# Optimization experiments

Measured on AMD Instinct MI355X. Metric: run time of the kernel, lower is better.

Reference implementation:

```python
import jax, jax.numpy as jnp
import numpy as np
from jax.scipy.special import logsumexp

B, T, V, E, F, H, L = 64, 512, 30000, 256, 256, 256, 9
DROPOUT_RATE, DROPOUT_ROUND = 0.1, 4


def setup_inputs() -> dict:
    key = jax.random.key(0)
    ks = jax.random.split(key, 20)
    lengths = jax.random.randint(ks[0], (B,), T // 2, T + 1)
    tok = jax.random.randint(ks[1], (B, T), 1, V)
    input_ids = jnp.where(jnp.arange(T)[None, :] < lengths[:, None], tok, 0).astype(jnp.int32)
    labels = jax.random.randint(ks[2], (B, T), 0, L).astype(jnp.int32)
    W_emb = (jax.random.normal(ks[3], (V, E)) * 0.1).at[0].set(0.0)  # padding_idx=0 row zeroed
    w0 = jax.random.normal(ks[4], (F, F, 3)) * 0.05
    w1 = jax.random.normal(ks[5], (F, F, 3)) * 0.05
    w2 = jax.random.normal(ks[6], (F, F, 3)) * 0.05
    Wl = jax.random.normal(ks[7], (E, F)) * 0.05
    Wh = jax.random.normal(ks[8], (F, H)) * 0.05
    Wfc = jax.random.normal(ks[9], (H, L)) * 0.05
    crf_start = jax.random.normal(ks[10], (L,)) * 0.1
    crf_end = jax.random.normal(ks[11], (L,)) * 0.1
    crf_trans = jax.random.normal(ks[12], (L, L)) * 0.1
    z = jnp.zeros
    return dict(input_ids=input_ids, labels=labels, W_emb=W_emb,
                w0=w0, b0=z((F,)), w1=w1, b1=z((F,)), w2=w2, b2=z((F,)),
                Wl=Wl, bl=z((F,)), Wh=Wh, bh=z((H,)), Wfc=Wfc, bfc=z((L,)),
                crf_start=crf_start, crf_end=crf_end, crf_trans=crf_trans)


def _conv1d(x, w, b, dil):
    # x: [B, C, T]; w: [O, I, K]; 'same' padding given kernel 3 / dilation
    pad = 1 + dil - 1  # kernel_size//2 + dilation - 1
    y = jax.lax.conv_general_dilated(x, w, window_strides=(1,), padding=[(pad, pad)],
                                     rhs_dilation=(dil,), dimension_numbers=('NCH', 'OIH', 'NCH'))
    return y + b[None, :, None]


def reference(input_ids, labels, W_emb, w0, b0, w1, b1, w2, b2,
              Wl, bl, Wh, bh, Wfc, bfc, crf_start, crf_end, crf_trans):
    mask = input_ids > 0  # [B,T] bool, mask[:,0] all True by construction

    # --- encoder: embedding + IDCNN ---
    emb = W_emb[input_ids]                       # [B,T,E]
    x = (emb @ Wl + bl).transpose(0, 2, 1)       # [B,F,T]

    def block(h):  # faithful to add_module name collision: conv0 -> relu -> conv1 -> conv2
        h = _conv1d(h, w0, b0, 1)
        h = jax.nn.relu(h)
        h = _conv1d(h, w1, b1, 1)
        h = _conv1d(h, w2, b2, 2)
        return h

    x = block(x)
    x = jax.nn.relu(x)
    x = block(x)
    x = block(x)
    x = block(x)

    out = x.transpose(0, 2, 1) @ Wh + bh         # [B,T,H]

    # --- multisample dropout + fc (deterministic masks via fixed keys) ---
    keep = 1.0 - DROPOUT_RATE
    logits = jnp.zeros((B, T, L), dtype=out.dtype)
    for r in range(DROPOUT_ROUND):
        m = jax.random.bernoulli(jax.random.fold_in(jax.random.key(42), r), keep, out.shape)
        logits = logits + ((out * m / keep) @ Wfc + bfc)
    logits = logits / DROPOUT_ROUND              # [B,T,L] emissions

    # --- CRF negative log-likelihood (reduction='sum') ---
    fmask = mask.astype(logits.dtype)

    # numerator: score of gold path
    emit_sc = jnp.take_along_axis(logits, labels[..., None], axis=-1)[..., 0]  # [B,T]
    trans_sc = crf_trans[labels[:, :-1], labels[:, 1:]]                        # [B,T-1]
    numer = crf_start[labels[:, 0]] + emit_sc[:, 0]
    numer = numer + jnp.sum((trans_sc + emit_sc[:, 1:]) * fmask[:, 1:], axis=1)
    seq_ends = jnp.sum(mask, axis=1).astype(jnp.int32) - 1
    last_tags = labels[jnp.arange(B), seq_ends]
    numer = numer + crf_end[last_tags]

    # denominator: forward algorithm (sequential scan over time)
    alpha0 = crf_start[None, :] + logits[:, 0]   # [B,L]

    def step(alpha, xs):
        em_t, m_t = xs                            # [B,L], [B]
        nxt = logsumexp(alpha[:, :, None] + crf_trans[None] + em_t[:, None, :], axis=1)
        alpha = jnp.where(m_t[:, None], nxt, alpha)
        return alpha, None

    alpha, _ = jax.lax.scan(step, alpha0, (logits[:, 1:].transpose(1, 0, 2), mask[:, 1:].T))
    denom = logsumexp(alpha + crf_end[None, :], axis=1)

    loss = jnp.sum(denom - numer)  # = -crf.llh(sum)
    return loss
```

## Files before the change

kernel.cpp:

```cpp
#include <hip/hip_runtime.h>
#include <stdint.h>

#define B_ 64
#define T_ 512
#define V_ 30000
#define E_ 256
#define F_ 256
#define H_ 256
#define L_ 9
#define TP_ 516
#define M_ (B_*T_)
#define HALF_ ((B_*T_*H_)/2)
#define NCHUNK_ 64
#define AELEM_ (132*32)
#define BELEM_ (3*128*32)

typedef float f32x4 __attribute__((ext_vector_type(4)));
typedef __bf16 bf16x8 __attribute__((ext_vector_type(8)));

typedef __attribute__((address_space(3))) unsigned int lds_uint;
typedef __attribute__((address_space(1))) const unsigned int glob_uint;

__device__ __forceinline__ unsigned short f2b(float f) {
  unsigned u = __float_as_uint(f);
  unsigned r = (u + 0x7FFFu + ((u >> 16) & 1u)) >> 16;
  return (unsigned short)r;
}
__device__ __forceinline__ unsigned pack2(float a, float b) {
  return (unsigned)f2b(a) | ((unsigned)f2b(b) << 16);
}

__device__ __forceinline__ void threefry2x32(unsigned k0, unsigned k1,
                                             unsigned x0, unsigned x1,
                                             unsigned &o0, unsigned &o1) {
  unsigned ks2 = k0 ^ k1 ^ 0x1BD11BDAu;
  x0 += k0; x1 += k1;
#define TFR(r) { x0 += x1; x1 = (x1 << r) | (x1 >> (32 - r)); x1 ^= x0; }
  TFR(13) TFR(15) TFR(26) TFR(6)   x0 += k1;  x1 += ks2 + 1u;
  TFR(17) TFR(29) TFR(16) TFR(24)  x0 += ks2; x1 += k0 + 2u;
  TFR(13) TFR(15) TFR(26) TFR(6)   x0 += k0;  x1 += k1 + 3u;
  TFR(17) TFR(29) TFR(16) TFR(24)  x0 += k1;  x1 += ks2 + 4u;
  TFR(13) TFR(15) TFR(26) TFR(6)   x0 += ks2; x1 += k0 + 5u;
#undef TFR
  o0 = x0; o1 = x1;
}

__global__ __launch_bounds__(256) void zero_pads(unsigned short* xb0, unsigned short* xb1) {
  int idx = blockIdx.x * 256 + threadIdx.x;
  int b = idx >> 10, rr = (idx >> 8) & 3, f = idx & 255;
  int row = (rr < 2) ? rr : 512 + rr;
  int o = (b * TP_ + row) * 256 + f;
  xb0[o] = 0; xb1[o] = 0;
}

__global__ __launch_bounds__(256) void prep_convw(const float* __restrict__ w,
                                                  unsigned short* __restrict__ BT) {
  int idx = blockIdx.x * 256 + threadIdx.x;
  if (idx < F_ * 768) {
    int o = idx / 768;
    int rem = idx - o * 768;
    int kk = rem >> 8;
    int i = rem & 255;
    BT[idx] = f2b(w[(o * 256 + i) * 3 + kk]);
  }
}

__global__ __launch_bounds__(256) void prep_mat(const float* __restrict__ Wm,
                                                unsigned short* __restrict__ BT) {
  int idx = blockIdx.x * 256 + threadIdx.x;
  int f = idx >> 8, e = idx & 255;
  BT[idx] = f2b(Wm[e * 256 + f]);
}

__global__ void foldkeys(unsigned* fk) {
  if (threadIdx.x == 0 && blockIdx.x == 0) {
    for (int r = 0; r < 4; ++r) {
      unsigned o0, o1;
      threefry2x32(0u, 42u, 0u, (unsigned)r, o0, o1);
      fk[2 * r] = o0; fk[2 * r + 1] = o1;
    }
  }
}

__global__ __launch_bounds__(256) void dropout_mask(const unsigned* __restrict__ fkg,
                                                    unsigned char* __restrict__ cnt) {
  unsigned fk0[4], fk1[4];
#pragma unroll
  for (int r = 0; r < 4; ++r) { fk0[r] = fkg[2 * r]; fk1[r] = fkg[2 * r + 1]; }
  const unsigned j0 = (blockIdx.x * 256 + threadIdx.x) * 4;
  unsigned c0 = 0, c1 = 0;
#pragma unroll
  for (int e = 0; e < 4; ++e) {
    unsigned a = 0, b = 0;
#pragma unroll
    for (int r = 0; r < 4; ++r) {
      unsigned o0, o1;
      threefry2x32(fk0[r], fk1[r], j0 + e, j0 + e + (unsigned)HALF_, o0, o1);
      a += (o0 < 0xE6666600u) ? 1u : 0u;
      b += (o1 < 0xE6666600u) ? 1u : 0u;
    }
    c0 |= a << (8 * e);
    c1 |= b << (8 * e);
  }
  *(unsigned*)(cnt + j0) = c0;
  *(unsigned*)(cnt + HALF_ + j0) = c1;
}

template<int DIL, bool RELU>
__global__ __launch_bounds__(256, 2)
void conv3_gemm(const unsigned short* __restrict__ xin,
                const unsigned short* __restrict__ BT,
                const float* __restrict__ bias,
                unsigned short* __restrict__ xout) {
  __shared__ unsigned short Al[2 * AELEM_];
  __shared__ unsigned short Bl[2 * BELEM_];
  const int tid = threadIdx.x;
  const int tm = blockIdx.x, tn = blockIdx.y;
  const int lane = tid & 63, wid = tid >> 6;
  const int wm = wid >> 1, wn = wid & 1;
  const int fr = lane & 15, fq = lane >> 4;

  const int r0 = tm * 128;
  const int bb0 = r0 >> 9, t0 = r0 & 511;
  const int pb = bb0 * TP_ + t0;

  int aoff[2];
#pragma unroll
  for (int s = 0; s < 2; ++s) {
    int c = s * 256 + tid;
    aoff[s] = (pb + (c >> 2)) * 256 + (c & 3) * 8;
  }
  const int hoff = (pb + 128 + (tid >> 2)) * 256 + (tid & 3) * 8;
  int boff[6];
#pragma unroll
  for (int s = 0; s < 6; ++s) {
    int c = s * 256 + tid;
    boff[s] = (tn * 128 + ((c >> 2) & 127)) * 768 + (c >> 9) * 256 + (c & 3) * 8;
  }
  const int aco[2] = {(0 * 256 + wid * 64) * 8, (1 * 256 + wid * 64) * 8};
  int bco[6];
#pragma unroll
  for (int s = 0; s < 6; ++s) bco[s] = (s * 256 + wid * 64) * 8;

  auto stage = [&](int p, int kin) {
    unsigned short* Ab = Al + p * AELEM_;
    unsigned short* Bb = Bl + p * BELEM_;
#pragma unroll
    for (int s = 0; s < 2; ++s)
      __builtin_amdgcn_global_load_lds((glob_uint*)(xin + aoff[s] + kin),
                                       (lds_uint*)(Ab + aco[s]), 16, 0, 0);
#pragma unroll
    for (int s = 0; s < 6; ++s)
      __builtin_amdgcn_global_load_lds((glob_uint*)(BT + boff[s] + kin),
                                       (lds_uint*)(Bb + bco[s]), 16, 0, 0);
    if (tid < 16)
      __builtin_amdgcn_global_load_lds((glob_uint*)(xin + hoff + kin),
                                       (lds_uint*)(Ab + 128 * 32), 16, 0, 0);
  };

  f32x4 acc[4][4] = {};

  stage(0, 0);
  __syncthreads();

  for (int ks = 0; ks < 8; ++ks) {
    const int cur = ks & 1;
    if (ks < 7) stage(cur ^ 1, (ks + 1) * 32);
    const unsigned short* Ab = Al + cur * AELEM_;
    const unsigned short* Bb = Bl + cur * BELEM_;
#pragma unroll
    for (int tp = 0; tp < 3; ++tp) {
      const int sh = (tp - 1) * DIL;
      bf16x8 af[4], bfv[4];
#pragma unroll
      for (int m = 0; m < 4; ++m)
        af[m] = *(const bf16x8*)(&Ab[(wm * 64 + m * 16 + fr + 2 + sh) * 32 + fq * 8]);
#pragma unroll
      for (int n = 0; n < 4; ++n)
        bfv[n] = *(const bf16x8*)(&Bb[(tp * 128 + wn * 64 + n * 16 + fr) * 32 + fq * 8]);
#pragma unroll
      for (int m = 0; m < 4; ++m)
#pragma unroll
        for (int n = 0; n < 4; ++n)
          acc[m][n] = __builtin_amdgcn_mfma_f32_16x16x32_bf16(af[m], bfv[n], acc[m][n], 0, 0, 0);
    }
    __syncthreads();
  }

#pragma unroll
  for (int n = 0; n < 4; ++n) {
    const int col = tn * 128 + wn * 64 + n * 16 + fr;
    const float bs = bias[col];
#pragma unroll
    for (int m = 0; m < 4; ++m) {
      const int row0 = tm * 128 + wm * 64 + m * 16 + fq * 4;
#pragma unroll
      for (int rg = 0; rg < 4; ++rg) {
        const int row = row0 + rg;
        float x = acc[m][n][rg] + bs;
        if (RELU) x = fmaxf(x, 0.f);
        int bb = row >> 9, t = row & 511;
        xout[(bb * TP_ + t + 2) * 256 + col] = f2b(x);
      }
    }
  }
}

__global__ __launch_bounds__(256, 2)
void head_lin(const unsigned short* __restrict__ xin,
              const unsigned short* __restrict__ BTh,
              const float* __restrict__ bh,
              float* __restrict__ outf) {
  __shared__ unsigned short Al[128 * 32];
  __shared__ unsigned short Bl[128 * 32];
  const int tid = threadIdx.x;
  const int tm = blockIdx.x, tn = blockIdx.y;
  const int lane = tid & 63, wid = tid >> 6;
  const int wm = wid >> 1, wn = wid & 1;
  const int fr = lane & 15, fq = lane >> 4;

  int aoff[2], boff[2];
#pragma unroll
  for (int s = 0; s < 2; ++s) {
    int c = s * 256 + tid;
    int rr = c >> 2, q = c & 3;
    int r = tm * 128 + rr;
    aoff[s] = ((r >> 9) * TP_ + (r & 511) + 2) * 256 + q * 8;
    boff[s] = (tn * 128 + rr) * 256 + q * 8;
  }
  unsigned short *ab[2], *bb[2];
#pragma unroll
  for (int s = 0; s < 2; ++s) {
    ab[s] = Al + (s * 256 + wid * 64) * 8;
    bb[s] = Bl + (s * 256 + wid * 64) * 8;
  }

  f32x4 acc[4][4] = {};

  for (int kin = 0; kin < 256; kin += 32) {
#pragma unroll
    for (int s = 0; s < 2; ++s) {
      __builtin_amdgcn_global_load_lds((glob_uint*)(xin + aoff[s] + kin),
                                       (lds_uint*)(ab[s]), 16, 0, 0);
      __builtin_amdgcn_global_load_lds((glob_uint*)(BTh + boff[s] + kin),
                                       (lds_uint*)(bb[s]), 16, 0, 0);
    }
    __syncthreads();
    bf16x8 af[4], bfv[4];
#pragma unroll
    for (int m = 0; m < 4; ++m)
      af[m] = *(const bf16x8*)(&Al[(wm * 64 + m * 16 + fr) * 32 + fq * 8]);
#pragma unroll
    for (int n = 0; n < 4; ++n)
      bfv[n] = *(const bf16x8*)(&Bl[(wn * 64 + n * 16 + fr) * 32 + fq * 8]);
#pragma unroll
    for (int m = 0; m < 4; ++m)
#pragma unroll
      for (int n = 0; n < 4; ++n)
        acc[m][n] = __builtin_amdgcn_mfma_f32_16x16x32_bf16(af[m], bfv[n], acc[m][n], 0, 0, 0);
    __syncthreads();
  }

#pragma unroll
  for (int n = 0; n < 4; ++n) {
    const int col = tn * 128 + wn * 64 + n * 16 + fr;
    const float bs = bh[col];
#pragma unroll
    for (int m = 0; m < 4; ++m) {
      const int row0 = tm * 128 + wm * 64 + m * 16 + fq * 4;
#pragma unroll
      for (int rg = 0; rg < 4; ++rg)
        outf[(size_t)(row0 + rg) * H_ + col] = acc[m][n][rg] + bs;
    }
  }
}

__global__ __launch_bounds__(256) void head_apply(const float* __restrict__ outf,
                                                  const unsigned char* __restrict__ cnt,
                                                  const float* __restrict__ Wfc,
                                                  const float* __restrict__ bfc,
                                                  float* __restrict__ logits) {
  __shared__ float sW[H_ * L_];
  __shared__ float sB[L_];
  int tid = threadIdx.x;
  for (int i = tid; i < H_ * L_; i += 256) sW[i] = Wfc[i];
  if (tid < L_) sB[tid] = bfc[tid];
  __syncthreads();
  const int lane = tid & 63, wid = tid >> 6;
  const int fr = lane & 15, g16 = lane >> 4;
  const int row = blockIdx.x * 16 + wid * 4 + g16;
  const float* orow = outf + (size_t)row * 256 + fr * 16;
  const unsigned char* crow = cnt + (size_t)row * 256 + fr * 16;
  uint4 cb = *(const uint4*)crow;
  const float sc = 1.0f / 3.6f;
  float a[9] = {};
#pragma unroll
  for (int q = 0; q < 4; ++q) {
    float4 v = *(const float4*)(orow + q * 4);
    unsigned cw = ((const unsigned*)&cb)[q];
    float xs[4] = {v.x, v.y, v.z, v.w};
#pragma unroll
    for (int k = 0; k < 4; ++k) {
      const int h = fr * 16 + q * 4 + k;
      const float x = xs[k] * (float)((cw >> (8 * k)) & 255u) * sc;
#pragma unroll
      for (int c = 0; c < 9; ++c) a[c] = fmaf(x, sW[h * 9 + c], a[c]);
    }
  }
#pragma unroll
  for (int c = 0; c < 9; ++c)
#pragma unroll
    for (int o = 1; o < 16; o <<= 1) a[c] += __shfl_xor(a[c], o);
  if (fr == 0) {
#pragma unroll
    for (int c = 0; c < 9; ++c) logits[(size_t)row * 9 + c] = a[c] + sB[c];
  }
}

__global__ __launch_bounds__(256) void crf_numer(const int* __restrict__ ids,
                                                 const int* __restrict__ labels,
                                                 const float* __restrict__ logits,
                                                 const float* __restrict__ cstart,
                                                 const float* __restrict__ cend,
                                                 const float* __restrict__ ctrans,
                                                 float* __restrict__ numer) {
  int b = blockIdx.x, tid = threadIdx.x;
  __shared__ float rs[256];
  __shared__ int rc[256];
  float p = 0.f; int cnt = 0;
  for (int t = tid; t < T_; t += 256) {
    int lab = labels[b * T_ + t];
    float em = logits[(b * T_ + t) * L_ + lab];
    int mk = ids[b * T_ + t] > 0;
    cnt += mk;
    if (t == 0) {
      p += cstart[lab] + em;
    } else if (mk) {
      int lp = labels[b * T_ + t - 1];
      p += ctrans[lp * L_ + lab] + em;
    }
  }
  rs[tid] = p; rc[tid] = cnt;
  __syncthreads();
  for (int s = 128; s > 0; s >>= 1) {
    if (tid < s) { rs[tid] += rs[tid + s]; rc[tid] += rc[tid + s]; }
    __syncthreads();
  }
  if (tid == 0) {
    int se = rc[0] - 1;
    int lt = labels[b * T_ + se];
    numer[b] = rs[0] + cend[lt];
  }
}

__global__ __launch_bounds__(128) void crf_chunk(const int* __restrict__ ids,
                                                 const float* __restrict__ logits,
                                                 const float* __restrict__ ctrans,
                                                 float* __restrict__ mats) {
  int blk = blockIdx.x;
  int b = blk >> 6, c = blk & 63;
  int e = threadIdx.x;
  int i = e / 9, j = e - 9 * i;
  __shared__ float cur[81];
  __shared__ float em[8 * 9];
  __shared__ int mk[8];
  int t0 = 8 * c;
  if (e < 72) em[e] = logits[((size_t)b * T_ + t0) * L_ + e];
  if (e < 8) mk[e] = (t0 + e >= 1) ? (ids[b * T_ + t0 + e] > 0) : 0;
  bool act = e < 81;
  float tcol[9];
  if (act) {
#pragma unroll
    for (int k = 0; k < 9; ++k) tcol[k] = ctrans[k * 9 + j];
    cur[e] = (i == j) ? 0.f : -1e30f;
  }
  __syncthreads();
  for (int s = 0; s < 8; ++s) {
    if (mk[s]) {
      float nv = 0.f;
      if (act) {
        float vv[9], mx = -3e38f;
#pragma unroll
        for (int k = 0; k < 9; ++k) { vv[k] = cur[i * 9 + k] + tcol[k]; mx = fmaxf(mx, vv[k]); }
        float ss = 0.f;
#pragma unroll
        for (int k = 0; k < 9; ++k) ss += __expf(vv[k] - mx);
        nv = mx + __logf(ss) + em[s * 9 + j];
      }
      __syncthreads();
      if (act) cur[e] = nv;
      __syncthreads();
    }
  }
  if (act) mats[(size_t)blk * 81 + e] = cur[e];
}

__global__ __launch_bounds__(256) void crf_combine(const float* __restrict__ mats,
                                                   const float* __restrict__ logits,
                                                   const float* __restrict__ cstart,
                                                   const float* __restrict__ cend,
                                                   const float* __restrict__ numer,
                                                   float* __restrict__ parts) {
  int b = blockIdx.x;
  __shared__ float bufA[64 * 81];
  __shared__ float bufB[32 * 81];
  __shared__ float alphaT[L_];
  int tid = threadIdx.x;
  for (int x = tid; x < 64 * 81; x += 256) bufA[x] = mats[(size_t)b * 64 * 81 + x];
  __syncthreads();
  float* src = bufA;
  float* dst = bufB;
  for (int n = 32; n >= 1; n >>= 1) {
    for (int x = tid; x < n * 81; x += 256) {
      int p = x / 81, e = x - 81 * p;
      int i = e / 9, j = e - 9 * i;
      const float* Lm = src + 162 * p;
      const float* Rm = Lm + 81;
      float vv[9], mx = -3e38f;
#pragma unroll
      for (int k = 0; k < 9; ++k) { vv[k] = Lm[i * 9 + k] + Rm[k * 9 + j]; mx = fmaxf(mx, vv[k]); }
      float ss = 0.f;
#pragma unroll
      for (int k = 0; k < 9; ++k) ss += __expf(vv[k] - mx);
      dst[x] = mx + __logf(ss);
    }
    __syncthreads();
    float* tmp = src; src = dst; dst = tmp;
  }
  const float* M = src;
  if (tid < L_) {
    int j = tid;
    float vv[9], mx = -3e38f;
#pragma unroll
    for (int i = 0; i < 9; ++i) {
      float a0 = cstart[i] + logits[(size_t)b * T_ * L_ + i];
      vv[i] = a0 + M[i * 9 + j];
      mx = fmaxf(mx, vv[i]);
    }
    float ss = 0.f;
#pragma unroll
    for (int i = 0; i < 9; ++i) ss += __expf(vv[i] - mx);
    alphaT[j] = mx + __logf(ss) + cend[j];
  }
  __syncthreads();
  if (tid == 0) {
    float mx = -3e38f;
#pragma unroll
    for (int j = 0; j < 9; ++j) mx = fmaxf(mx, alphaT[j]);
    float ss = 0.f;
#pragma unroll
    for (int j = 0; j < 9; ++j) ss += __expf(alphaT[j] - mx);
    parts[b] = mx + __logf(ss) - numer[b];
  }
}

__global__ void final_reduce(const float* __restrict__ parts, float* __restrict__ out) {
  int tid = threadIdx.x;
  float v = parts[tid];
#pragma unroll
  for (int off = 32; off; off >>= 1) v += __shfl_down(v, off);
  if (tid == 0) out[0] = v;
}

__global__ __launch_bounds__(256, 2)
void embed_gemm(const int* __restrict__ ids,
                const float* __restrict__ Wemb,
                const unsigned short* __restrict__ BT,
                const float* __restrict__ bias,
                unsigned short* __restrict__ xout) {
  __shared__ unsigned short Al[128 * 40];
  __shared__ unsigned short Bl[128 * 40];
  const int tid = threadIdx.x;
  const int tm = blockIdx.x, tn = blockIdx.y;
  const int lane = tid & 63, wid = tid >> 6;
  const int wm = wid >> 1, wn = wid & 1;
  const int fr = lane & 15, fq = lane >> 4;

  int asrc[2], boff[2], loff[2];
#pragma unroll
  for (int it = 0; it < 2; ++it) {
    int e = it * 256 + tid;
    int row = e >> 2, kq = e & 3;
    int r = tm * 128 + row;
    asrc[it] = ids[r] * E_ + kq * 8;
    boff[it] = (tn * 128 + row) * E_ + kq * 8;
    loff[it] = row * 40 + kq * 8;
  }

  f32x4 acc[4][4] = {};

  for (int k0 = 0; k0 < E_; k0 += 32) {
#pragma unroll
    for (int it = 0; it < 2; ++it) {
      const float* s = Wemb + asrc[it] + k0;
      float4 v0 = *(const float4*)s;
      float4 v1 = *(const float4*)(s + 4);
      uint4 va;
      va.x = pack2(v0.x, v0.y); va.y = pack2(v0.z, v0.w);
      va.z = pack2(v1.x, v1.y); va.w = pack2(v1.z, v1.w);
      uint4 vb = *(const uint4*)(BT + boff[it] + k0);
      *(uint4*)(&Al[loff[it]]) = va;
      *(uint4*)(&Bl[loff[it]]) = vb;
    }
    __syncthreads();
    bf16x8 af[4], bfv[4];
#pragma unroll
    for (int m = 0; m < 4; ++m)
      af[m] = *(const bf16x8*)(&Al[(wm * 64 + m * 16 + fr) * 40 + fq * 8]);
#pragma unroll
    for (int n = 0; n < 4; ++n)
      bfv[n] = *(const bf16x8*)(&Bl[(wn * 64 + n * 16 + fr) * 40 + fq * 8]);
#pragma unroll
    for (int m = 0; m < 4; ++m)
#pragma unroll
      for (int n = 0; n < 4; ++n)
        acc[m][n] = __builtin_amdgcn_mfma_f32_16x16x32_bf16(af[m], bfv[n], acc[m][n], 0, 0, 0);
    __syncthreads();
  }

#pragma unroll
  for (int n = 0; n < 4; ++n) {
    const int col = tn * 128 + wn * 64 + n * 16 + fr;
    const float bs = bias[col];
#pragma unroll
    for (int m = 0; m < 4; ++m) {
      const int row0 = tm * 128 + wm * 64 + m * 16 + fq * 4;
#pragma unroll
      for (int rg = 0; rg < 4; ++rg) {
        const int row = row0 + rg;
        float x = acc[m][n][rg] + bs;
        int bb = row >> 9, t = row & 511;
        xout[(bb * TP_ + t + 2) * 256 + col] = f2b(x);
      }
    }
  }
}

extern "C" void kernel_launch(void* const* d_in, const int* in_sizes, int n_in,
                              void* d_out, int out_size, void* d_ws, size_t ws_size,
                              hipStream_t stream) {
  const int*   ids    = (const int*)d_in[0];
  const int*   labels = (const int*)d_in[1];
  const float* Wemb   = (const float*)d_in[2];
  const float* w0     = (const float*)d_in[3];
  const float* b0     = (const float*)d_in[4];
  const float* w1     = (const float*)d_in[5];
  const float* b1     = (const float*)d_in[6];
  const float* w2     = (const float*)d_in[7];
  const float* b2     = (const float*)d_in[8];
  const float* Wl     = (const float*)d_in[9];
  const float* bl     = (const float*)d_in[10];
  const float* Wh     = (const float*)d_in[11];
  const float* bh     = (const float*)d_in[12];
  const float* Wfc    = (const float*)d_in[13];
  const float* bfc    = (const float*)d_in[14];
  const float* cstart = (const float*)d_in[15];
  const float* cend   = (const float*)d_in[16];
  const float* ctrans = (const float*)d_in[17];

  char* ws = (char*)d_ws;
  size_t off = 0;
  auto alloc = [&](size_t bytes) -> void* {
    void* p = ws + off;
    off += (bytes + 255) & ~(size_t)255;
    return p;
  };
  unsigned short* xb0 = (unsigned short*)alloc((size_t)B_ * TP_ * F_ * 2);
  unsigned short* xb1 = (unsigned short*)alloc((size_t)B_ * TP_ * F_ * 2);
  unsigned short* BTl = (unsigned short*)alloc((size_t)E_ * F_ * 2);
  unsigned short* BT0 = (unsigned short*)alloc((size_t)F_ * 768 * 2);
  unsigned short* BT1 = (unsigned short*)alloc((size_t)F_ * 768 * 2);
  unsigned short* BT2 = (unsigned short*)alloc((size_t)F_ * 768 * 2);
  unsigned short* BTh = (unsigned short*)alloc((size_t)F_ * H_ * 2);
  float* outf   = (float*)alloc((size_t)M_ * H_ * 4);
  unsigned char* cntb = (unsigned char*)alloc((size_t)M_ * H_);
  float* logits = (float*)alloc((size_t)M_ * L_ * 4);
  unsigned* fk  = (unsigned*)alloc(64);
  float* numer  = (float*)alloc(B_ * 4);
  float* parts  = (float*)alloc(B_ * 4);
  float* mats   = (float*)alloc((size_t)B_ * NCHUNK_ * 81 * 4);
  if (ws_size < off) return;

  zero_pads<<<256, 256, 0, stream>>>(xb0, xb1);
  prep_convw<<<768, 256, 0, stream>>>(w0, BT0);
  prep_convw<<<768, 256, 0, stream>>>(w1, BT1);
  prep_convw<<<768, 256, 0, stream>>>(w2, BT2);
  prep_mat<<<256, 256, 0, stream>>>(Wl, BTl);
  prep_mat<<<256, 256, 0, stream>>>(Wh, BTh);
  foldkeys<<<1, 64, 0, stream>>>(fk);
  dropout_mask<<<HALF_ / 1024, 256, 0, stream>>>(fk, cntb);

  dim3 grid(M_ / 128, F_ / 128);
  embed_gemm<<<grid, 256, 0, stream>>>(ids, Wemb, BTl, bl, xb0);

  conv3_gemm<1, true ><<<grid, 256, 0, stream>>>(xb0, BT0, b0, xb1);
  conv3_gemm<1, false><<<grid, 256, 0, stream>>>(xb1, BT1, b1, xb0);
  conv3_gemm<2, true ><<<grid, 256, 0, stream>>>(xb0, BT2, b2, xb1);
  conv3_gemm<1, true ><<<grid, 256, 0, stream>>>(xb1, BT0, b0, xb0);
  conv3_gemm<1, false><<<grid, 256, 0, stream>>>(xb0, BT1, b1, xb1);
  conv3_gemm<2, false><<<grid, 256, 0, stream>>>(xb1, BT2, b2, xb0);
  conv3_gemm<1, true ><<<grid, 256, 0, stream>>>(xb0, BT0, b0, xb1);
  conv3_gemm<1, false><<<grid, 256, 0, stream>>>(xb1, BT1, b1, xb0);
  conv3_gemm<2, false><<<grid, 256, 0, stream>>>(xb0, BT2, b2, xb1);
  conv3_gemm<1, true ><<<grid, 256, 0, stream>>>(xb1, BT0, b0, xb0);
  conv3_gemm<1, false><<<grid, 256, 0, stream>>>(xb0, BT1, b1, xb1);
  conv3_gemm<2, false><<<grid, 256, 0, stream>>>(xb1, BT2, b2, xb0);

  head_lin<<<grid, 256, 0, stream>>>(xb0, BTh, bh, outf);
  head_apply<<<M_ / 16, 256, 0, stream>>>(outf, cntb, Wfc, bfc, logits);

  crf_numer<<<B_, 256, 0, stream>>>(ids, labels, logits, cstart, cend, ctrans, numer);
  crf_chunk<<<B_ * NCHUNK_, 128, 0, stream>>>(ids, logits, ctrans, mats);
  crf_combine<<<B_, 256, 0, stream>>>(mats, logits, cstart, cend, numer, parts);
  final_reduce<<<1, 64, 0, stream>>>(parts, (float*)d_out);
}
```

Baseline: 341.8 us.

## Store head activations as bf16 and single-buffer conv GEMM LDS staging

The head linear layer now writes its output as bf16 rather than fp32, and head_apply reads and unpacks the bf16 values. This halves the traffic of the large intermediate between the two head kernels, at the cost of an extra rounding step before dropout and the FC layer. Separately, conv3_gemm drops its double-buffered LDS staging and uses a single buffer: load, sync, compute, sync. This cuts shared memory per block but removes the overlap between global-to-LDS loads and MFMA work in the twelve conv launches.

```diff
diff --git a/kernel.cpp b/kernel.cpp
--- a/kernel.cpp
+++ b/kernel.cpp
@@ -12,8 +12,6 @@
 #define M_ (B_*T_)
 #define HALF_ ((B_*T_*H_)/2)
 #define NCHUNK_ 64
-#define AELEM_ (132*32)
-#define BELEM_ (3*128*32)
 
 typedef float f32x4 __attribute__((ext_vector_type(4)));
 typedef __bf16 bf16x8 __attribute__((ext_vector_type(8)));
@@ -28,6 +26,9 @@
 }
 __device__ __forceinline__ unsigned pack2(float a, float b) {
   return (unsigned)f2b(a) | ((unsigned)f2b(b) << 16);
+}
+__device__ __forceinline__ float b2f(unsigned short u) {
+  return __uint_as_float(((unsigned)u) << 16);
 }
 
 __device__ __forceinline__ void threefry2x32(unsigned k0, unsigned k1,
@@ -112,8 +113,8 @@
                 const unsigned short* __restrict__ BT,
                 const float* __restrict__ bias,
                 unsigned short* __restrict__ xout) {
-  __shared__ unsigned short Al[2 * AELEM_];
-  __shared__ unsigned short Bl[2 * BELEM_];
+  __shared__ unsigned short Al[132 * 32];
+  __shared__ unsigned short Bl[3 * 128 * 32];
   const int tid = threadIdx.x;
   const int tm = blockIdx.x, tn = blockIdx.y;
   const int lane = tid & 63, wid = tid >> 6;
@@ -137,47 +138,38 @@
     int c = s * 256 + tid;
     boff[s] = (tn * 128 + ((c >> 2) & 127)) * 768 + (c >> 9) * 256 + (c & 3) * 8;
   }
-  const int aco[2] = {(0 * 256 + wid * 64) * 8, (1 * 256 + wid * 64) * 8};
-  int bco[6];
-#pragma unroll
-  for (int s = 0; s < 6; ++s) bco[s] = (s * 256 + wid * 64) * 8;
-
-  auto stage = [&](int p, int kin) {
-    unsigned short* Ab = Al + p * AELEM_;
-    unsigned short* Bb = Bl + p * BELEM_;
+  unsigned short* abase[2];
+  unsigned short* bbase[6];
+#pragma unroll
+  for (int s = 0; s < 2; ++s) abase[s] = Al + (s * 256 + wid * 64) * 8;
+#pragma unroll
+  for (int s = 0; s < 6; ++s) bbase[s] = Bl + (s * 256 + wid * 64) * 8;
+
+  f32x4 acc[4][4] = {};
+
+  for (int kin = 0; kin < 256; kin += 32) {
 #pragma unroll
     for (int s = 0; s < 2; ++s)
       __builtin_amdgcn_global_load_lds((glob_uint*)(xin + aoff[s] + kin),
-                                       (lds_uint*)(Ab + aco[s]), 16, 0, 0);
+                                       (lds_uint*)(abase[s]), 16, 0, 0);
 #pragma unroll
     for (int s = 0; s < 6; ++s)
       __builtin_amdgcn_global_load_lds((glob_uint*)(BT + boff[s] + kin),
-                                       (lds_uint*)(Bb + bco[s]), 16, 0, 0);
+                                       (lds_uint*)(bbase[s]), 16, 0, 0);
     if (tid < 16)
       __builtin_amdgcn_global_load_lds((glob_uint*)(xin + hoff + kin),
-                                       (lds_uint*)(Ab + 128 * 32), 16, 0, 0);
-  };
-
-  f32x4 acc[4][4] = {};
-
-  stage(0, 0);
-  __syncthreads();
-
-  for (int ks = 0; ks < 8; ++ks) {
-    const int cur = ks & 1;
-    if (ks < 7) stage(cur ^ 1, (ks + 1) * 32);
-    const unsigned short* Ab = Al + cur * AELEM_;
-    const unsigned short* Bb = Bl + cur * BELEM_;
+                                       (lds_uint*)(Al + 128 * 32), 16, 0, 0);
+    __syncthreads();
 #pragma unroll
     for (int tp = 0; tp < 3; ++tp) {
       const int sh = (tp - 1) * DIL;
       bf16x8 af[4], bfv[4];
 #pragma unroll
       for (int m = 0; m < 4; ++m)
-        af[m] = *(const bf16x8*)(&Ab[(wm * 64 + m * 16 + fr + 2 + sh) * 32 + fq * 8]);
+        af[m] = *(const bf16x8*)(&Al[(wm * 64 + m * 16 + fr + 2 + sh) * 32 + fq * 8]);
 #pragma unroll
       for (int n = 0; n < 4; ++n)
-        bfv[n] = *(const bf16x8*)(&Bb[(tp * 128 + wn * 64 + n * 16 + fr) * 32 + fq * 8]);
+        bfv[n] = *(const bf16x8*)(&Bl[(tp * 128 + wn * 64 + n * 16 + fr) * 32 + fq * 8]);
 #pragma unroll
       for (int m = 0; m < 4; ++m)
 #pragma unroll
@@ -210,7 +202,7 @@
 void head_lin(const unsigned short* __restrict__ xin,
               const unsigned short* __restrict__ BTh,
               const float* __restrict__ bh,
-              float* __restrict__ outf) {
+              unsigned short* __restrict__ outh) {
   __shared__ unsigned short Al[128 * 32];
   __shared__ unsigned short Bl[128 * 32];
   const int tid = threadIdx.x;
@@ -270,12 +262,12 @@
       const int row0 = tm * 128 + wm * 64 + m * 16 + fq * 4;
 #pragma unroll
       for (int rg = 0; rg < 4; ++rg)
-        outf[(size_t)(row0 + rg) * H_ + col] = acc[m][n][rg] + bs;
-    }
-  }
-}
-
-__global__ __launch_bounds__(256) void head_apply(const float* __restrict__ outf,
+        outh[(size_t)(row0 + rg) * H_ + col] = f2b(acc[m][n][rg] + bs);
+    }
+  }
+}
+
+__global__ __launch_bounds__(256) void head_apply(const unsigned short* __restrict__ outh,
                                                   const unsigned char* __restrict__ cnt,
                                                   const float* __restrict__ Wfc,
                                                   const float* __restrict__ bfc,
@@ -289,16 +281,24 @@
   const int lane = tid & 63, wid = tid >> 6;
   const int fr = lane & 15, g16 = lane >> 4;
   const int row = blockIdx.x * 16 + wid * 4 + g16;
-  const float* orow = outf + (size_t)row * 256 + fr * 16;
+  const unsigned short* orow = outh + (size_t)row * 256 + fr * 16;
   const unsigned char* crow = cnt + (size_t)row * 256 + fr * 16;
+  uint4 ob0 = *(const uint4*)orow;
+  uint4 ob1 = *(const uint4*)(orow + 8);
   uint4 cb = *(const uint4*)crow;
   const float sc = 1.0f / 3.6f;
   float a[9] = {};
+  const unsigned* ow = (const unsigned*)&ob0;
 #pragma unroll
   for (int q = 0; q < 4; ++q) {
-    float4 v = *(const float4*)(orow + q * 4);
+    unsigned w0 = (q < 2) ? ((const unsigned*)&ob0)[2 * q]     : ((const unsigned*)&ob1)[2 * (q - 2)];
+    unsigned w1 = (q < 2) ? ((const unsigned*)&ob0)[2 * q + 1] : ((const unsigned*)&ob1)[2 * (q - 2) + 1];
     unsigned cw = ((const unsigned*)&cb)[q];
-    float xs[4] = {v.x, v.y, v.z, v.w};
+    float xs[4];
+    xs[0] = __uint_as_float(w0 << 16);
+    xs[1] = __uint_as_float(w0 & 0xFFFF0000u);
+    xs[2] = __uint_as_float(w1 << 16);
+    xs[3] = __uint_as_float(w1 & 0xFFFF0000u);
 #pragma unroll
     for (int k = 0; k < 4; ++k) {
       const int h = fr * 16 + q * 4 + k;
@@ -307,6 +307,7 @@
       for (int c = 0; c < 9; ++c) a[c] = fmaf(x, sW[h * 9 + c], a[c]);
     }
   }
+  (void)ow;
 #pragma unroll
   for (int c = 0; c < 9; ++c)
 #pragma unroll
@@ -572,7 +573,7 @@
   unsigned short* BT1 = (unsigned short*)alloc((size_t)F_ * 768 * 2);
   unsigned short* BT2 = (unsigned short*)alloc((size_t)F_ * 768 * 2);
   unsigned short* BTh = (unsigned short*)alloc((size_t)F_ * H_ * 2);
-  float* outf   = (float*)alloc((size_t)M_ * H_ * 4);
+  unsigned short* outh = (unsigned short*)alloc((size_t)M_ * H_ * 2);
   unsigned char* cntb = (unsigned char*)alloc((size_t)M_ * H_);
   float* logits = (float*)alloc((size_t)M_ * L_ * 4);
   unsigned* fk  = (unsigned*)alloc(64);
@@ -606,8 +607,8 @@
   conv3_gemm<1, false><<<grid, 256, 0, stream>>>(xb0, BT1, b1, xb1);
   conv3_gemm<2, false><<<grid, 256, 0, stream>>>(xb1, BT2, b2, xb0);
 
-  head_lin<<<grid, 256, 0, stream>>>(xb0, BTh, bh, outf);
-  head_apply<<<M_ / 16, 256, 0, stream>>>(outf, cntb, Wfc, bfc, logits);
+  head_lin<<<grid, 256, 0, stream>>>(xb0, BTh, bh, outh);
+  head_apply<<<M_ / 16, 256, 0, stream>>>(outh, cntb, Wfc, bfc, logits);
 
   crf_numer<<<B_, 256, 0, stream>>>(ids, labels, logits, cstart, cend, ctrans, numer);
   crf_chunk<<<B_ * NCHUNK_, 128, 0, stream>>>(ids, logits, ctrans, mats);
```

Measured after the change: 351.3 us. +2.8%, slower.
